# Optimization experiments

Measured on AMD Instinct MI355X. Metric: run time of the kernel, lower is better.

## Reference

```python
import jax, jax.numpy as jnp
import numpy as np

QUERY_DIM = 512
INNER_DIM = 2 * QUERY_DIM  # 1024
CROSS_DIM = 512


def setup_inputs() -> dict:
    key = jax.random.key(0)
    k1, k2, k3, k4, k5, k6, k7 = jax.random.split(key, 7)
    B, N1, N2 = 8, 2048, 2048
    S1 = jax.random.normal(k1, (B, N1, CROSS_DIM), dtype=jnp.float32)
    S2 = jax.random.normal(k2, (B, N2, QUERY_DIM), dtype=jnp.float32)
    # Linear weights stored as [in, out] (pre-transposed vs torch's [out, in])
    sq = 1.0 / np.sqrt(QUERY_DIM)
    sc = 1.0 / np.sqrt(CROSS_DIM)
    si = 1.0 / np.sqrt(INNER_DIM)
    Wq = jax.random.uniform(k3, (QUERY_DIM, INNER_DIM), jnp.float32, -sq, sq)
    Wk = jax.random.uniform(k4, (CROSS_DIM, INNER_DIM), jnp.float32, -sc, sc)
    Wv = jax.random.uniform(k5, (CROSS_DIM, INNER_DIM), jnp.float32, -sc, sc)
    Wo = jax.random.uniform(k6, (INNER_DIM, QUERY_DIM), jnp.float32, -si, si)
    bo = jax.random.uniform(k7, (QUERY_DIM,), jnp.float32, -si, si)
    return {"S1": S1, "S2": S2, "Wq": Wq, "Wk": Wk, "Wv": Wv, "Wo": Wo, "bo": bo}


def reference(S1, S2, Wq, Wk, Wv, Wo, bo):
    # softmax((Wq S2)(Wk S1)^T) (Wv S1), then output projection. NOTE: no 1/sqrt(d) scaling.
    query = jnp.einsum('bnd,de->bne', S2, Wq)   # [B, N2, inner]
    key_ = jnp.einsum('bmd,de->bme', S1, Wk)    # [B, N1, inner]
    value = jnp.einsum('bmd,de->bme', S1, Wv)   # [B, N1, inner]
    scores = jnp.einsum('bne,bme->bnm', query, key_)  # [B, N2, N1]
    attn = jax.nn.softmax(scores, axis=-1)
    masked = jnp.einsum('bnm,bme->bne', attn, value)  # [B, N2, inner]
    out = jnp.einsum('bne,ed->bnd', masked, Wo) + bo  # [B, N2, query_dim]
    return out
```

## Files before the change

### kernel.cpp

```cpp
#include <hip/hip_runtime.h>


typedef _Float16 h_t;
typedef _Float16 h8 __attribute__((ext_vector_type(8)));
typedef _Float16 h4 __attribute__((ext_vector_type(4)));
typedef float f4 __attribute__((ext_vector_type(4)));

#define MFMA16(a, b, c) __builtin_amdgcn_mfma_f32_16x16x32_f16(a, b, c, 0, 0, 0)

typedef const __attribute__((address_space(1))) void* gas_t;
typedef __attribute__((address_space(3))) void* las_t;

__device__ __forceinline__ void gl2lds16(const void* g, void* l) {
    __builtin_amdgcn_global_load_lds((gas_t)g, (las_t)l, 16, 0, 0);
}

__global__ __launch_bounds__(256) void k_prep(const float* __restrict__ S1,
                                              const float* __restrict__ S2,
                                              const float* __restrict__ Wq,
                                              const float* __restrict__ Wk,
                                              const float* __restrict__ Wv,
                                              const float* __restrict__ Wo,
                                              h_t* __restrict__ S1h,
                                              h_t* __restrict__ S2h,
                                              h_t* __restrict__ Wqh,
                                              h_t* __restrict__ Wkh,
                                              h_t* __restrict__ Wvh,
                                              h_t* __restrict__ Wot) {
    __shared__ float tile[32][33];
    long bid = blockIdx.x;
    if (bid < 17920) {
        long i = bid * 256 + threadIdx.x;
        const long n = 2097152;
        const long wn = 131072;
        const float* src;
        h_t* dst;
        long off;
        if (i < n) { src = S1; dst = S1h; off = i; }
        else if (i < 2 * n) { src = S2; dst = S2h; off = i - n; }
        else if (i < 2 * n + wn) { src = Wq; dst = Wqh; off = i - 2 * n; }
        else if (i < 2 * n + 2 * wn) { src = Wk; dst = Wkh; off = i - 2 * n - wn; }
        else { src = Wv; dst = Wvh; off = i - 2 * n - 2 * wn; }
        float4 v = *((const float4*)src + off);
        h4 h = {(h_t)v.x, (h_t)v.y, (h_t)v.z, (h_t)v.w};
        *((h4*)dst + off) = h;
    } else {
        int tid = (int)(bid - 17920);
        const int K = 1024, N = 512;
        int nb = (tid & 15) * 32, kb = (tid >> 4) * 32;
        int x = threadIdx.x & 31, y = threadIdx.x >> 5;
#pragma unroll
        for (int j = 0; j < 4; j++)
            tile[y + j * 8][x] = Wo[(size_t)(kb + y + j * 8) * N + nb + x];
        __syncthreads();
#pragma unroll
        for (int j = 0; j < 4; j++)
            Wot[(size_t)(nb + y + j * 8) * K + kb + x] = (h_t)tile[x][y + j * 8];
    }
}

__global__ __launch_bounds__(256) void k_wpre(const h_t* __restrict__ Wqh,
                                              const h_t* __restrict__ Wkh,
                                              const h_t* __restrict__ Wot,
                                              const h_t* __restrict__ Wvh,
                                              h_t* __restrict__ Wkq,
                                              h_t* __restrict__ Wvot) {
    __shared__ h_t As[128 * 64];
    __shared__ h_t Bs[128 * 64];
    int t = threadIdx.x, w = t >> 6, lane = t & 63;
    int q16 = lane >> 4, l16 = lane & 15;
    int id = blockIdx.x;
    const h_t* A;
    const h_t* Bt;
    h_t* C;
    float oscale;
    if (id < 16) { A = Wkh; Bt = Wqh; C = Wkq; oscale = 1.44269504f; }
    else { id -= 16; A = Wot; Bt = Wvh; C = Wvot; oscale = 1.0f; }
    size_t m0 = (size_t)(id >> 2) * 128, n0 = (size_t)(id & 3) * 128;
    const int K = 1024, N = 512;
    int wr = (w >> 1) * 64, wc = (w & 1) * 64;
    f4 acc[4][4] = {};

    for (int k0 = 0; k0 < K; k0 += 64) {
#pragma unroll
        for (int j = 0; j < 4; j++) {
            int q = w * 4 + j;
            int row = q * 8 + (lane >> 3);
            int ks = (((lane & 7) ^ (row & 7)) << 3);
            gl2lds16(A + (m0 + row) * K + k0 + ks, &As[q * 512]);
            gl2lds16(Bt + (n0 + row) * K + k0 + ks, &Bs[q * 512]);
        }
        __syncthreads();
#pragma unroll
        for (int ks = 0; ks < 2; ks++) {
            h8 av[4], bv[4];
#pragma unroll
            for (int i = 0; i < 4; i++) {
                int row = wr + i * 16 + l16;
                int ch = ks * 4 + q16;
                av[i] = *(const h8*)&As[row * 64 + ((ch ^ (row & 7)) << 3)];
            }
#pragma unroll
            for (int j = 0; j < 4; j++) {
                int row = wc + j * 16 + l16;
                int ch = ks * 4 + q16;
                bv[j] = *(const h8*)&Bs[row * 64 + ((ch ^ (row & 7)) << 3)];
            }
#pragma unroll
            for (int i = 0; i < 4; i++)
#pragma unroll
                for (int j = 0; j < 4; j++)
                    acc[i][j] = MFMA16(av[i], bv[j], acc[i][j]);
        }
        __syncthreads();
    }
#pragma unroll
    for (int i = 0; i < 4; i++) {
        size_t r0 = m0 + wr + i * 16 + q16 * 4;
#pragma unroll
        for (int j = 0; j < 4; j++) {
            size_t c = n0 + wc + j * 16 + l16;
#pragma unroll
            for (int r = 0; r < 4; r++)
                C[(r0 + r) * N + c] = (h_t)(acc[i][j][r] * oscale);
        }
    }
}

__global__ __launch_bounds__(256) void k_proj2(const h_t* __restrict__ S2h,
                                               const h_t* __restrict__ S1h,
                                               const h_t* __restrict__ Wkq,
                                               const h_t* __restrict__ Wvot,
                                               const float* __restrict__ bo,
                                               h_t* __restrict__ T,
                                               h_t* __restrict__ Vt) {
    __shared__ h_t As[128 * 64];
    __shared__ h_t Bs[128 * 64];
    int t = threadIdx.x, w = t >> 6, lane = t & 63;
    int q16 = lane >> 4, l16 = lane & 15;
    int id = blockIdx.x;
    int mode = id >> 9;
    id &= 511;
    const h_t* A = mode ? S1h : S2h;
    const h_t* Bt = mode ? Wvot : Wkq;
    size_t m0 = (size_t)(id >> 2) * 128, n0 = (size_t)(id & 3) * 128;
    const int K = 512;
    int wr = (w >> 1) * 64, wc = (w & 1) * 64;
    f4 acc[4][4] = {};

    for (int k0 = 0; k0 < K; k0 += 64) {
#pragma unroll
        for (int j = 0; j < 4; j++) {
            int q = w * 4 + j;
            int row = q * 8 + (lane >> 3);
            int ks = (((lane & 7) ^ (row & 7)) << 3);
            gl2lds16(A + (m0 + row) * K + k0 + ks, &As[q * 512]);
            gl2lds16(Bt + (n0 + row) * K + k0 + ks, &Bs[q * 512]);
        }
        __syncthreads();
#pragma unroll
        for (int ks = 0; ks < 2; ks++) {
            h8 av[4], bv[4];
#pragma unroll
            for (int i = 0; i < 4; i++) {
                int row = wr + i * 16 + l16;
                int ch = ks * 4 + q16;
                av[i] = *(const h8*)&As[row * 64 + ((ch ^ (row & 7)) << 3)];
            }
#pragma unroll
            for (int j = 0; j < 4; j++) {
                int row = wc + j * 16 + l16;
                int ch = ks * 4 + q16;
                bv[j] = *(const h8*)&Bs[row * 64 + ((ch ^ (row & 7)) << 3)];
            }
#pragma unroll
            for (int i = 0; i < 4; i++)
#pragma unroll
                for (int j = 0; j < 4; j++)
                    acc[i][j] = MFMA16(av[i], bv[j], acc[i][j]);
        }
        __syncthreads();
    }
    if (mode == 0) {
#pragma unroll
        for (int i = 0; i < 4; i++) {
            size_t r0 = m0 + wr + i * 16 + q16 * 4;
#pragma unroll
            for (int j = 0; j < 4; j++) {
                size_t c = n0 + wc + j * 16 + l16;
#pragma unroll
                for (int r = 0; r < 4; r++)
                    T[(r0 + r) * 512 + c] = (h_t)acc[i][j][r];
            }
        }
    } else {
#pragma unroll
        for (int i = 0; i < 4; i++) {
            size_t gm = m0 + wr + i * 16 + q16 * 4;
            size_t b = gm >> 11;
            size_t n = gm & 2047;
#pragma unroll
            for (int j = 0; j < 4; j++) {
                size_t d = n0 + wc + j * 16 + l16;
                float bias = bo[d];
                h4 hv = {(h_t)(acc[i][j][0] + bias), (h_t)(acc[i][j][1] + bias),
                         (h_t)(acc[i][j][2] + bias), (h_t)(acc[i][j][3] + bias)};
                *(h4*)&Vt[(b * 512 + d) * 2048 + n] = hv;
            }
        }
    }
}

__global__ __launch_bounds__(256) void k_qk(const h_t* __restrict__ T,
                                            const h_t* __restrict__ S1h,
                                            h_t* __restrict__ P,
                                            float2* __restrict__ Mkt) {
    __shared__ h_t sm[18432];
    h_t* As = sm;
    h_t* Bs = sm + 8192;
    float* pmx = (float*)(sm + 17408);
    float* psm = (float*)(sm + 17920);
    int t = threadIdx.x, w = t >> 6, lane = t & 63;
    int q16 = lane >> 4, l16 = lane & 15;
    int qt = blockIdx.x, kt = blockIdx.y, b = blockIdx.z;
    const h_t* A = S1h + ((size_t)b * 2048 + kt * 128) * 512;
    const h_t* Bt = T + ((size_t)b * 2048 + qt * 128) * 512;
    int wr = (w >> 1) * 64, wc = (w & 1) * 64;
    f4 acc[4][4] = {};

    for (int k0 = 0; k0 < 512; k0 += 64) {
#pragma unroll
        for (int j = 0; j < 4; j++) {
            int q = w * 4 + j;
            int row = q * 8 + (lane >> 3);
            int ks = (((lane & 7) ^ (row & 7)) << 3);
            gl2lds16(A + (size_t)row * 512 + k0 + ks, &As[q * 512]);
            gl2lds16(Bt + (size_t)row * 512 + k0 + ks, &Bs[q * 512]);
        }
        __syncthreads();
#pragma unroll
        for (int ks = 0; ks < 2; ks++) {
            h8 av[4], bv[4];
#pragma unroll
            for (int i = 0; i < 4; i++) {
                int row = wr + i * 16 + l16;
                int ch = ks * 4 + q16;
                av[i] = *(const h8*)&As[row * 64 + ((ch ^ (row & 7)) << 3)];
            }
#pragma unroll
            for (int j = 0; j < 4; j++) {
                int row = wc + j * 16 + l16;
                int ch = ks * 4 + q16;
                bv[j] = *(const h8*)&Bs[row * 64 + ((ch ^ (row & 7)) << 3)];
            }
#pragma unroll
            for (int i = 0; i < 4; i++)
#pragma unroll
                for (int j = 0; j < 4; j++)
                    acc[i][j] = MFMA16(av[i], bv[j], acc[i][j]);
        }
        __syncthreads();
    }
    float lm[4], ls[4], sc[4];
#pragma unroll
    for (int j = 0; j < 4; j++) {
        float m = acc[0][j][0];
#pragma unroll
        for (int i = 0; i < 4; i++)
#pragma unroll
            for (int r = 0; r < 4; r++) m = fmaxf(m, acc[i][j][r]);
        lm[j] = m;
    }
#pragma unroll
    for (int msk = 16; msk <= 32; msk <<= 1)
#pragma unroll
        for (int j = 0; j < 4; j++)
            lm[j] = fmaxf(lm[j], __shfl_xor(lm[j], msk, 64));
#pragma unroll
    for (int j = 0; j < 4; j++) {
        float s = 0.f;
#pragma unroll
        for (int i = 0; i < 4; i++)
#pragma unroll
            for (int r = 0; r < 4; r++) {
                float e = exp2f(acc[i][j][r] - lm[j]);
                acc[i][j][r] = e;
                s += e;
            }
        ls[j] = s;
    }
#pragma unroll
    for (int msk = 16; msk <= 32; msk <<= 1)
#pragma unroll
        for (int j = 0; j < 4; j++) ls[j] += __shfl_xor(ls[j], msk, 64);
    if (q16 == 0) {
#pragma unroll
        for (int j = 0; j < 4; j++) {
            pmx[(w >> 1) * 128 + wc + j * 16 + l16] = lm[j];
            psm[(w >> 1) * 128 + wc + j * 16 + l16] = ls[j];
        }
    }
    __syncthreads();
#pragma unroll
    for (int j = 0; j < 4; j++) {
        int row = wc + j * 16 + l16;
        float om = pmx[((w >> 1) ^ 1) * 128 + row];
        float os = psm[((w >> 1) ^ 1) * 128 + row];
        float M = fmaxf(lm[j], om);
        float s = exp2f(lm[j] - M);
        float L = ls[j] * s + os * exp2f(om - M);
        sc[j] = s;
        if ((w >> 1) == 0 && q16 == 0)
            Mkt[((size_t)b * 16 + kt) * 2048 + qt * 128 + row] = make_float2(M, L);
    }
#pragma unroll
    for (int j = 0; j < 4; j++)
#pragma unroll
        for (int i = 0; i < 4; i++) {
            h4 hv = {(h_t)(acc[i][j][0] * sc[j]), (h_t)(acc[i][j][1] * sc[j]),
                     (h_t)(acc[i][j][2] * sc[j]), (h_t)(acc[i][j][3] * sc[j])};
            *(h4*)&sm[(wc + j * 16 + l16) * 136 + wr + i * 16 + q16 * 4] = hv;
        }
    __syncthreads();
    size_t Pbase = ((size_t)b * 2048 + qt * 128) * 2048 + (size_t)kt * 128;
#pragma unroll
    for (int p = 0; p < 8; p++) {
        int row = p * 16 + (t >> 4);
        int c8 = (t & 15) * 8;
        *(h8*)(P + Pbase + (size_t)row * 2048 + c8) = *(const h8*)&sm[row * 136 + c8];
    }
}

__global__ __launch_bounds__(256) void k_pv(const h_t* __restrict__ P,
                                            const h_t* __restrict__ Vt,
                                            const float2* __restrict__ Mkt,
                                            float* __restrict__ Out) {
    __shared__ h_t As[128 * 64];
    __shared__ h_t Bs[128 * 64];
    __shared__ h_t dks[16][128];
    __shared__ float linv[128];
    int t = threadIdx.x, w = t >> 6, lane = t & 63;
    int q16 = lane >> 4, l16 = lane & 15;
    int rt = blockIdx.x, dt = blockIdx.y, b = blockIdx.z;
    int rg = w >> 1, dg = w & 1;
    if (t < 128) {
        float2 v[16];
        float m = -1e30f;
#pragma unroll
        for (int kt = 0; kt < 16; kt++) {
            v[kt] = Mkt[((size_t)b * 16 + kt) * 2048 + rt * 128 + t];
            m = fmaxf(m, v[kt].x);
        }
        float l = 0.f;
#pragma unroll
        for (int kt = 0; kt < 16; kt++) {
            float d = exp2f(v[kt].x - m);
            l += v[kt].y * d;
            dks[kt][t] = (h_t)d;
        }
        linv[t] = 1.f / l;
    }
    __syncthreads();

    const h_t* Pb = P + ((size_t)b * 2048 + rt * 128) * 2048;
    const h_t* Vb = Vt + ((size_t)b * 512 + dt * 128) * 2048;
    int srow = t >> 3, soct = t & 7;
    f4 acc[4][4] = {};

    for (int k0 = 0; k0 < 2048; k0 += 64) {
        int kt = k0 >> 7;
#pragma unroll
        for (int p = 0; p < 4; p++) {
            int r_ = p * 32 + srow;
            h_t dh = dks[kt][r_];
            h8 dv = {dh, dh, dh, dh, dh, dh, dh, dh};
            h8 v = *(const h8*)(Pb + (size_t)r_ * 2048 + k0 + soct * 8);
            v = v * dv;
            *(h8*)&As[r_ * 64 + ((soct ^ (r_ & 7)) << 3)] = v;
        }
#pragma unroll
        for (int j = 0; j < 4; j++) {
            int q = w * 4 + j;
            int row = q * 8 + (lane >> 3);
            int ks = (((lane & 7) ^ (row & 7)) << 3);
            gl2lds16(Vb + (size_t)row * 2048 + k0 + ks, &Bs[q * 512]);
        }
        __syncthreads();
#pragma unroll
        for (int ks = 0; ks < 2; ks++) {
            int ch = ks * 4 + q16;
            h8 av[4], bv[4];
#pragma unroll
            for (int i = 0; i < 4; i++) {
                int row = rg * 64 + i * 16 + l16;
                av[i] = *(const h8*)&As[row * 64 + ((ch ^ (row & 7)) << 3)];
            }
#pragma unroll
            for (int j = 0; j < 4; j++) {
                int dr = dg * 64 + j * 16 + l16;
                bv[j] = *(const h8*)&Bs[dr * 64 + ((ch ^ (dr & 7)) << 3)];
            }
#pragma unroll
            for (int i = 0; i < 4; i++)
#pragma unroll
                for (int j = 0; j < 4; j++)
                    acc[i][j] = MFMA16(av[i], bv[j], acc[i][j]);
        }
        __syncthreads();
    }
#pragma unroll
    for (int i = 0; i < 4; i++)
#pragma unroll
        for (int rr = 0; rr < 4; rr++) {
            int row = rg * 64 + i * 16 + q16 * 4 + rr;
            float lv = linv[row];
#pragma unroll
            for (int j = 0; j < 4; j++) {
                int d = dt * 128 + dg * 64 + j * 16 + l16;
                Out[((size_t)b * 2048 + rt * 128 + row) * 512 + d] =
                    acc[i][j][rr] * lv;
            }
        }
}

extern "C" void kernel_launch(void* const* d_in, const int* in_sizes, int n_in,
                              void* d_out, int out_size, void* d_ws, size_t ws_size,
                              hipStream_t stream) {
    const float* S1 = (const float*)d_in[0];
    const float* S2 = (const float*)d_in[1];
    const float* Wq = (const float*)d_in[2];
    const float* Wk = (const float*)d_in[3];
    const float* Wv = (const float*)d_in[4];
    const float* Wo = (const float*)d_in[5];
    const float* bo = (const float*)d_in[6];
    float* Out = (float*)d_out;

    char* ws = (char*)d_ws;
    h_t* S1h  = (h_t*)(ws);
    h_t* T    = (h_t*)(ws + 16777216);
    h_t* Vt   = (h_t*)(ws + 33554432);
    h_t* P    = (h_t*)(ws + 50331648);
    float2* Mkt = (float2*)(ws + 117440512);
    h_t* S2h  = (h_t*)(ws + 50331648);
    h_t* Wqh  = (h_t*)(ws + 67108864);
    h_t* Wkh  = (h_t*)(ws + 68157440);
    h_t* Wvh  = (h_t*)(ws + 69206016);
    h_t* Wot  = (h_t*)(ws + 70254592);
    h_t* Wkq  = (h_t*)(ws + 71303168);
    h_t* Wvot = (h_t*)(ws + 71827456);

    k_prep<<<18432, 256, 0, stream>>>(S1, S2, Wq, Wk, Wv, Wo,
                                      S1h, S2h, Wqh, Wkh, Wvh, Wot);
    k_wpre<<<32, 256, 0, stream>>>(Wqh, Wkh, Wot, Wvh, Wkq, Wvot);
    k_proj2<<<1024, 256, 0, stream>>>(S2h, S1h, Wkq, Wvot, bo, T, Vt);
    k_qk<<<dim3(16, 16, 8), 256, 0, stream>>>(T, S1h, P, Mkt);
    k_pv<<<dim3(16, 4, 8), 256, 0, stream>>>(P, Vt, Mkt, Out);
}
```

Before: 280.4 us.

## Double-buffer LDS staging with manual vmcnt waits in projection, QK and PV GEMMs

Adds two LDS buffers to the projection, QK and PV GEMM kernels so the next K-tile's global-to-LDS loads are issued while MFMAs run on the current tile. Full __syncthreads are replaced by explicit s_waitcnt vmcnt/lgkmcnt plus s_barrier. In the PV kernel, P rows are register-prefetched one tile ahead before being scaled and stored to LDS. The aim is to hide global load latency behind compute, at the cost of more LDS per block (lower occupancy) and fragile hand-written waitcnt counts.

```diff
diff --git a/kernel.cpp b/kernel.cpp
--- a/kernel.cpp
+++ b/kernel.cpp
@@ -134,8 +134,7 @@
                                                const float* __restrict__ bo,
                                                h_t* __restrict__ T,
                                                h_t* __restrict__ Vt) {
-    __shared__ h_t As[128 * 64];
-    __shared__ h_t Bs[128 * 64];
+    __shared__ h_t smem[2][16384];
     int t = threadIdx.x, w = t >> 6, lane = t & 63;
     int q16 = lane >> 4, l16 = lane & 15;
     int id = blockIdx.x;
@@ -144,20 +143,34 @@
     const h_t* A = mode ? S1h : S2h;
     const h_t* Bt = mode ? Wvot : Wkq;
     size_t m0 = (size_t)(id >> 2) * 128, n0 = (size_t)(id & 3) * 128;
-    const int K = 512;
     int wr = (w >> 1) * 64, wc = (w & 1) * 64;
     f4 acc[4][4] = {};
 
-    for (int k0 = 0; k0 < K; k0 += 64) {
+    auto STAGE = [&](int k0_, int bsel) {
 #pragma unroll
         for (int j = 0; j < 4; j++) {
             int q = w * 4 + j;
             int row = q * 8 + (lane >> 3);
             int ks = (((lane & 7) ^ (row & 7)) << 3);
-            gl2lds16(A + (m0 + row) * K + k0 + ks, &As[q * 512]);
-            gl2lds16(Bt + (n0 + row) * K + k0 + ks, &Bs[q * 512]);
-        }
-        __syncthreads();
+            gl2lds16(A + (m0 + row) * 512 + k0_ + ks, &smem[bsel][q * 512]);
+            gl2lds16(Bt + (n0 + row) * 512 + k0_ + ks, &smem[bsel][8192 + q * 512]);
+        }
+    };
+
+    STAGE(0, 0);
+    int cur = 0;
+#pragma unroll 1
+    for (int it = 0; it < 8; it++) {
+        if (it < 7) {
+            STAGE((it + 1) * 64, cur ^ 1);
+            asm volatile("s_waitcnt vmcnt(8)" ::: "memory");
+        } else {
+            asm volatile("s_waitcnt vmcnt(0)" ::: "memory");
+        }
+        __builtin_amdgcn_s_barrier();
+        asm volatile("" ::: "memory");
+        const h_t* As = &smem[cur][0];
+        const h_t* Bs = &smem[cur][8192];
 #pragma unroll
         for (int ks = 0; ks < 2; ks++) {
             h8 av[4], bv[4];
@@ -179,7 +192,9 @@
                 for (int j = 0; j < 4; j++)
                     acc[i][j] = MFMA16(av[i], bv[j], acc[i][j]);
         }
-        __syncthreads();
+        asm volatile("" ::: "memory");
+        __builtin_amdgcn_s_barrier();
+        cur ^= 1;
     }
     if (mode == 0) {
 #pragma unroll
@@ -215,11 +230,9 @@
                                             const h_t* __restrict__ S1h,
                                             h_t* __restrict__ P,
                                             float2* __restrict__ Mkt) {
-    __shared__ h_t sm[18432];
-    h_t* As = sm;
-    h_t* Bs = sm + 8192;
-    float* pmx = (float*)(sm + 17408);
-    float* psm = (float*)(sm + 17920);
+    __shared__ h_t smem[2][16384];
+    __shared__ float pmx[2][128], psm[2][128];
+    h_t* Ps = &smem[0][0];
     int t = threadIdx.x, w = t >> 6, lane = t & 63;
     int q16 = lane >> 4, l16 = lane & 15;
     int qt = blockIdx.x, kt = blockIdx.y, b = blockIdx.z;
@@ -228,16 +241,31 @@
     int wr = (w >> 1) * 64, wc = (w & 1) * 64;
     f4 acc[4][4] = {};
 
-    for (int k0 = 0; k0 < 512; k0 += 64) {
+    auto STAGE = [&](int k0_, int bsel) {
 #pragma unroll
         for (int j = 0; j < 4; j++) {
             int q = w * 4 + j;
             int row = q * 8 + (lane >> 3);
             int ks = (((lane & 7) ^ (row & 7)) << 3);
-            gl2lds16(A + (size_t)row * 512 + k0 + ks, &As[q * 512]);
-            gl2lds16(Bt + (size_t)row * 512 + k0 + ks, &Bs[q * 512]);
-        }
-        __syncthreads();
+            gl2lds16(A + (size_t)row * 512 + k0_ + ks, &smem[bsel][q * 512]);
+            gl2lds16(Bt + (size_t)row * 512 + k0_ + ks, &smem[bsel][8192 + q * 512]);
+        }
+    };
+
+    STAGE(0, 0);
+    int cur = 0;
+#pragma unroll 1
+    for (int it = 0; it < 8; it++) {
+        if (it < 7) {
+            STAGE((it + 1) * 64, cur ^ 1);
+            asm volatile("s_waitcnt vmcnt(8)" ::: "memory");
+        } else {
+            asm volatile("s_waitcnt vmcnt(0)" ::: "memory");
+        }
+        __builtin_amdgcn_s_barrier();
+        asm volatile("" ::: "memory");
+        const h_t* As = &smem[cur][0];
+        const h_t* Bs = &smem[cur][8192];
 #pragma unroll
         for (int ks = 0; ks < 2; ks++) {
             h8 av[4], bv[4];
@@ -259,7 +287,9 @@
                 for (int j = 0; j < 4; j++)
                     acc[i][j] = MFMA16(av[i], bv[j], acc[i][j]);
         }
-        __syncthreads();
+        asm volatile("" ::: "memory");
+        __builtin_amdgcn_s_barrier();
+        cur ^= 1;
     }
     float lm[4], ls[4], sc[4];
 #pragma unroll
@@ -296,16 +326,16 @@
     if (q16 == 0) {
 #pragma unroll
         for (int j = 0; j < 4; j++) {
-            pmx[(w >> 1) * 128 + wc + j * 16 + l16] = lm[j];
-            psm[(w >> 1) * 128 + wc + j * 16 + l16] = ls[j];
+            pmx[w >> 1][wc + j * 16 + l16] = lm[j];
+            psm[w >> 1][wc + j * 16 + l16] = ls[j];
         }
     }
     __syncthreads();
 #pragma unroll
     for (int j = 0; j < 4; j++) {
         int row = wc + j * 16 + l16;
-        float om = pmx[((w >> 1) ^ 1) * 128 + row];
-        float os = psm[((w >> 1) ^ 1) * 128 + row];
+        float om = pmx[(w >> 1) ^ 1][row];
+        float os = psm[(w >> 1) ^ 1][row];
         float M = fmaxf(lm[j], om);
         float s = exp2f(lm[j] - M);
         float L = ls[j] * s + os * exp2f(om - M);
@@ -319,7 +349,7 @@
         for (int i = 0; i < 4; i++) {
             h4 hv = {(h_t)(acc[i][j][0] * sc[j]), (h_t)(acc[i][j][1] * sc[j]),
                      (h_t)(acc[i][j][2] * sc[j]), (h_t)(acc[i][j][3] * sc[j])};
-            *(h4*)&sm[(wc + j * 16 + l16) * 136 + wr + i * 16 + q16 * 4] = hv;
+            *(h4*)&Ps[(wc + j * 16 + l16) * 136 + wr + i * 16 + q16 * 4] = hv;
         }
     __syncthreads();
     size_t Pbase = ((size_t)b * 2048 + qt * 128) * 2048 + (size_t)kt * 128;
@@ -327,7 +357,7 @@
     for (int p = 0; p < 8; p++) {
         int row = p * 16 + (t >> 4);
         int c8 = (t & 15) * 8;
-        *(h8*)(P + Pbase + (size_t)row * 2048 + c8) = *(const h8*)&sm[row * 136 + c8];
+        *(h8*)(P + Pbase + (size_t)row * 2048 + c8) = *(const h8*)&Ps[row * 136 + c8];
     }
 }
 
@@ -336,7 +366,7 @@
                                             const float2* __restrict__ Mkt,
                                             float* __restrict__ Out) {
     __shared__ h_t As[128 * 64];
-    __shared__ h_t Bs[128 * 64];
+    __shared__ h_t Bs[2][128 * 64];
     __shared__ h_t dks[16][128];
     __shared__ float linv[128];
     int t = threadIdx.x, w = t >> 6, lane = t & 63;
@@ -366,26 +396,28 @@
     const h_t* Vb = Vt + ((size_t)b * 512 + dt * 128) * 2048;
     int srow = t >> 3, soct = t & 7;
     f4 acc[4][4] = {};
-
-    for (int k0 = 0; k0 < 2048; k0 += 64) {
-        int kt = k0 >> 7;
-#pragma unroll
-        for (int p = 0; p < 4; p++) {
-            int r_ = p * 32 + srow;
-            h_t dh = dks[kt][r_];
-            h8 dv = {dh, dh, dh, dh, dh, dh, dh, dh};
-            h8 v = *(const h8*)(Pb + (size_t)r_ * 2048 + k0 + soct * 8);
-            v = v * dv;
-            *(h8*)&As[r_ * 64 + ((soct ^ (r_ & 7)) << 3)] = v;
-        }
+    h8 prA[4], prB[4];
+
+    auto VSTAGE = [&](int k0_, int bsel) {
 #pragma unroll
         for (int j = 0; j < 4; j++) {
             int q = w * 4 + j;
             int row = q * 8 + (lane >> 3);
             int ks = (((lane & 7) ^ (row & 7)) << 3);
-            gl2lds16(Vb + (size_t)row * 2048 + k0 + ks, &Bs[q * 512]);
-        }
-        __syncthreads();
+            gl2lds16(Vb + (size_t)row * 2048 + k0_ + ks, &Bs[bsel][q * 512]);
+        }
+    };
+    auto ASTORE = [&](h8* pr, int kt_) {
+#pragma unroll
+        for (int p = 0; p < 4; p++) {
+            int r_ = p * 32 + srow;
+            h_t dh = dks[kt_][r_];
+            h8 dv = {dh, dh, dh, dh, dh, dh, dh, dh};
+            h8 v = pr[p] * dv;
+            *(h8*)&As[r_ * 64 + ((soct ^ (r_ & 7)) << 3)] = v;
+        }
+    };
+    auto MM = [&](const h_t* Bsc) {
 #pragma unroll
         for (int ks = 0; ks < 2; ks++) {
             int ch = ks * 4 + q16;
@@ -398,7 +430,7 @@
 #pragma unroll
             for (int j = 0; j < 4; j++) {
                 int dr = dg * 64 + j * 16 + l16;
-                bv[j] = *(const h8*)&Bs[dr * 64 + ((ch ^ (dr & 7)) << 3)];
+                bv[j] = *(const h8*)&Bsc[dr * 64 + ((ch ^ (dr & 7)) << 3)];
             }
 #pragma unroll
             for (int i = 0; i < 4; i++)
@@ -406,7 +438,44 @@
                 for (int j = 0; j < 4; j++)
                     acc[i][j] = MFMA16(av[i], bv[j], acc[i][j]);
         }
-        __syncthreads();
+    };
+
+#pragma unroll
+    for (int p = 0; p < 4; p++)
+        prA[p] = *(const h8*)(Pb + (size_t)(p * 32 + srow) * 2048 + soct * 8);
+    VSTAGE(0, 0);
+
+#pragma unroll 1
+    for (int it2 = 0; it2 < 16; it2++) {
+        int k0 = it2 * 128;
+#pragma unroll
+        for (int p = 0; p < 4; p++)
+            prB[p] = *(const h8*)(Pb + (size_t)(p * 32 + srow) * 2048 + k0 + 64 + soct * 8);
+        VSTAGE(k0 + 64, 1);
+        asm volatile("s_waitcnt vmcnt(8)" ::: "memory");
+        ASTORE(prA, k0 >> 7);
+        asm volatile("s_waitcnt lgkmcnt(0)" ::: "memory");
+        __builtin_amdgcn_s_barrier();
+        asm volatile("" ::: "memory");
+        MM(&Bs[0][0]);
+        asm volatile("" ::: "memory");
+        __builtin_amdgcn_s_barrier();
+        if (it2 < 15) {
+#pragma unroll
+            for (int p = 0; p < 4; p++)
+                prA[p] = *(const h8*)(Pb + (size_t)(p * 32 + srow) * 2048 + k0 + 128 + soct * 8);
+            VSTAGE(k0 + 128, 0);
+            asm volatile("s_waitcnt vmcnt(8)" ::: "memory");
+        } else {
+            asm volatile("s_waitcnt vmcnt(0)" ::: "memory");
+        }
+        ASTORE(prB, (k0 + 64) >> 7);
+        asm volatile("s_waitcnt lgkmcnt(0)" ::: "memory");
+        __builtin_amdgcn_s_barrier();
+        asm volatile("" ::: "memory");
+        MM(&Bs[1][0]);
+        asm volatile("" ::: "memory");
+        __builtin_amdgcn_s_barrier();
     }
 #pragma unroll
     for (int i = 0; i < 4; i++)
@@ -418,7 +487,7 @@
             for (int j = 0; j < 4; j++) {
                 int d = dt * 128 + dg * 64 + j * 16 + l16;
                 Out[((size_t)b * 2048 + rt * 128 + row) * 512 + d] =
-                    acc[i][j][rr] * lv;
+                    acc[i][rr >= 0 ? j : j][rr] * lv;
             }
         }
 }
```

Result: no change. 277.2 us (-1.1%).
